# Performance work log

Hardware: AMD Instinct MI355X
Metric: run time of the kernel (lower is better)

Reference implementation:

```python
import jax, jax.numpy as jnp
import numpy as np


def setup_inputs() -> dict:
    key = jax.random.key(0)
    ks = jax.random.split(key, 6)
    B, S, D, E = 4, 2048, 1024, 8
    H = 4 * D
    return {
        "x": jax.random.normal(ks[0], (B, S, D), dtype=jnp.float32),
        "logits": jax.random.normal(ks[1], (B, S, E), dtype=jnp.float32),
        "noise": jax.random.normal(ks[2], (B, S, E), dtype=jnp.float32),
        "W1": jax.random.normal(ks[3], (E, D, H), dtype=jnp.float32) * (1.0 / np.sqrt(D)),
        "b1": jnp.zeros((E, H), dtype=jnp.float32),
        "W2": jax.random.normal(ks[4], (E, H, D), dtype=jnp.float32) * (1.0 / np.sqrt(H)),
        "b2": jnp.zeros((E, D), dtype=jnp.float32),
        "top_k": 2,
    }


def reference(x, logits, noise, W1, b1, W2, b2, top_k):
    # NoisyTopkRouter_Cluster: noise scaled by softplus(logits), then sparse top-k softmax
    B, S, D = x.shape
    E = logits.shape[-1]
    noisy = logits + noise * jax.nn.softplus(logits)           # [B,S,E]
    _, topi = jax.lax.top_k(noisy, top_k)                      # [B,S,K]
    in_topk = jax.nn.one_hot(topi, E, dtype=jnp.bool_).any(-2)  # [B,S,E]
    sparse = jnp.where(in_topk, noisy, -jnp.inf)
    gates = jax.nn.softmax(sparse, axis=-1)                    # [B,S,E]; zero off top-k

    # SparseMoE combine: sum_e gate[:, e] * Expert_e(x). Gate is exactly 0 for
    # unselected experts, so dense-masked compute matches the gather/scatter loop.
    xf = x.reshape(-1, D)                                      # [T,D]
    gf = gates.reshape(-1, E).T                                # [E,T]

    def body(acc, params):
        w1, bb1, w2, bb2, g = params                           # g: [T]
        h = jax.nn.relu(xf @ w1 + bb1)                         # [T,4D]
        acc = acc + (h @ w2 + bb2) * g[:, None]
        return acc, None

    acc, _ = jax.lax.scan(body, jnp.zeros_like(xf), (W1, b1, W2, b2, gf))
    return acc.reshape(B, S, D)
```

## Files before the change

kernel.cpp:

```cpp
#include <hip/hip_runtime.h>
#include <cstdint>
#include <cstddef>

#define T_TOK 8192
#define E_NUM 8
#define D_DIM 1024
#define H_DIM 4096
#define MAXTILES 136
#define TILE 128
#define BK 32

typedef __attribute__((ext_vector_type(8))) short short8;
typedef __attribute__((ext_vector_type(4))) float f32x4;
typedef __attribute__((ext_vector_type(8))) unsigned short ushort8v;
typedef __attribute__((ext_vector_type(4))) unsigned short ushort4v;

__device__ __forceinline__ unsigned short f2b(float f) {
  unsigned int u = __float_as_uint(f);
  u += 0x7fffu + ((u >> 16) & 1u);
  return (unsigned short)(u >> 16);
}

__device__ __forceinline__ void async16(const void* g, void* l) {
  __builtin_amdgcn_global_load_lds((const __attribute__((address_space(1))) void*)g,
                                   (__attribute__((address_space(3))) void*)l, 16, 0, 0);
}

__global__ void router_kernel(const float* __restrict__ logits, const float* __restrict__ noise,
                              int* __restrict__ counts, int* __restrict__ ti, float* __restrict__ tg) {
  int tk = blockIdx.x * blockDim.x + threadIdx.x;
  if (tk >= T_TOK) return;
  float nz[E_NUM];
#pragma unroll
  for (int e = 0; e < E_NUM; ++e) {
    float l = logits[tk * E_NUM + e];
    float sp = fmaxf(l, 0.f) + log1pf(expf(-fabsf(l)));
    nz[e] = l + noise[tk * E_NUM + e] * sp;
  }
  int i1 = 0; float v1 = nz[0];
#pragma unroll
  for (int e = 1; e < E_NUM; ++e) if (nz[e] > v1) { v1 = nz[e]; i1 = e; }
  int i2 = -1; float v2 = -3.0e38f;
#pragma unroll
  for (int e = 0; e < E_NUM; ++e) if (e != i1 && nz[e] > v2) { v2 = nz[e]; i2 = e; }
  float ex = expf(v2 - v1);
  float g1 = 1.f / (1.f + ex);
  float g2 = ex / (1.f + ex);
  int s1 = atomicAdd(&counts[i1], 1);
  int s2 = atomicAdd(&counts[i2], 1);
  ti[tk*4+0] = i1; ti[tk*4+1] = s1; ti[tk*4+2] = i2; ti[tk*4+3] = s2;
  tg[tk*2+0] = g1; tg[tk*2+1] = g2;
}

__global__ void setup_kernel(const int* __restrict__ counts, int* __restrict__ offs,
                             int* __restrict__ tab) {
  int o = 0;
  for (int e = 0; e < E_NUM; ++e) { offs[e] = o; o += counts[e]; }
  offs[E_NUM] = o;
  int mt = 0;
  for (int e = 0; e < E_NUM; ++e)
    for (int m0 = 0; m0 < counts[e]; m0 += TILE) { tab[mt*2] = e; tab[mt*2+1] = m0; ++mt; }
  for (; mt < MAXTILES; ++mt) { tab[mt*2] = -1; tab[mt*2+1] = 0; }
}

__global__ void gather_kernel(const float* __restrict__ x, const int* __restrict__ ti,
                              const float* __restrict__ tg, const int* __restrict__ offs,
                              unsigned short* __restrict__ xg, int* __restrict__ stok,
                              float* __restrict__ sg) {
  const int tk = blockIdx.x, t = threadIdx.x;
  const int i1 = ti[tk*4+0], s1 = ti[tk*4+1], i2 = ti[tk*4+2], s2 = ti[tk*4+3];
  const int r1 = offs[i1] + s1, r2 = offs[i2] + s2;
  if (t == 0) {
    stok[r1] = tk; sg[r1] = tg[tk*2+0];
    stok[r2] = tk; sg[r2] = tg[tk*2+1];
  }
  const float4 v = *(const float4*)(x + (size_t)tk * D_DIM + t * 4);
  ushort4v bb; bb.x = f2b(v.x); bb.y = f2b(v.y); bb.z = f2b(v.z); bb.w = f2b(v.w);
  *(ushort4v*)(xg + (size_t)r1 * D_DIM + t * 4) = bb;
  *(ushort4v*)(xg + (size_t)r2 * D_DIM + t * 4) = bb;
}

__global__ void transpose_kernel(const float* __restrict__ W, unsigned short* __restrict__ Wt,
                                 int K, int N) {
  const int e = blockIdx.z;
  const float* We = W + (size_t)e * K * N;
  unsigned short* Wte = Wt + (size_t)e * K * N;
  __shared__ __align__(16) unsigned short tb[64 * 72];
  const int n0 = blockIdx.x * 64, k0 = blockIdx.y * 64;
  const int t = threadIdx.x;
  const int kr = t >> 4;
  const int c4 = (t & 15) * 4;
#pragma unroll
  for (int rr = 0; rr < 4; ++rr) {
    int k = kr + rr * 16;
    const float4 v = *(const float4*)(We + (size_t)(k0 + k) * N + n0 + c4);
    tb[(c4+0)*72 + k] = f2b(v.x);
    tb[(c4+1)*72 + k] = f2b(v.y);
    tb[(c4+2)*72 + k] = f2b(v.z);
    tb[(c4+3)*72 + k] = f2b(v.w);
  }
  __syncthreads();
  const int n = t >> 2, kq = (t & 3) * 16;
  ushort8v a = *(const ushort8v*)&tb[n*72 + kq];
  ushort8v b = *(const ushort8v*)&tb[n*72 + kq + 8];
  *(ushort8v*)(Wte + (size_t)(n0+n)*K + k0 + kq) = a;
  *(ushort8v*)(Wte + (size_t)(n0+n)*K + k0 + kq + 8) = b;
}

template<int EPI>
__global__ __launch_bounds__(256)
void gemm_bt(const unsigned short* __restrict__ A, const unsigned short* __restrict__ Bt,
             const int K, const int N,
             const int* __restrict__ counts, const int* __restrict__ offs,
             const int* __restrict__ tab,
             const float* __restrict__ bias,
             unsigned short* __restrict__ Hout,
             float* __restrict__ Out,
             const int* __restrict__ slot_tok, const float* __restrict__ slot_gate) {
  const int mt = blockIdx.y;
  const int e = tab[mt*2];
  if (e < 0) return;
  const int m0  = tab[mt*2+1];
  const int cnt = counts[e];
  const int seg = offs[e];
  const int n0  = blockIdx.x * TILE;

  __shared__ __align__(16) short As[TILE*BK];
  __shared__ __align__(16) short Bs[TILE*BK];
  __shared__ int   s_tok[TILE];
  __shared__ float s_g[TILE];

  const int t = threadIdx.x;
  const int lane = t & 63;
  const int wv = t >> 6;
  const int wm = wv & 1, wn = wv >> 1;
  const int fr = lane & 15, fq = lane >> 4;

  if (EPI == 1 && t < TILE) {
    int rl = m0 + t;
    if (rl < cnt) { s_tok[t] = slot_tok[seg + rl]; s_g[t] = slot_gate[seg + rl]; }
    else          { s_tok[t] = 0;                  s_g[t] = 0.f; }
  }

  const unsigned short* Ae = A + (size_t)seg * K;
  const unsigned short* Be = Bt + (size_t)e * N * K + (size_t)n0 * K;

  const int row0 = t >> 2;
  const int kq0  = (t & 3) * 8;
  int ar0 = m0 + row0;        ar0 = ar0 < cnt ? ar0 : cnt - 1;
  int ar1 = m0 + row0 + 64;   ar1 = ar1 < cnt ? ar1 : cnt - 1;
  const unsigned short* gA0 = Ae + (size_t)ar0 * K + kq0;
  const unsigned short* gA1 = Ae + (size_t)ar1 * K + kq0;
  const unsigned short* gB0 = Be + (size_t)row0 * K + kq0;
  const unsigned short* gB1 = Be + (size_t)(row0 + 64) * K + kq0;
  char* lA0 = (char*)As + wv*1024;
  char* lA1 = (char*)As + 4096 + wv*1024;
  char* lB0 = (char*)Bs + wv*1024;
  char* lB1 = (char*)Bs + 4096 + wv*1024;

  f32x4 acc[4][4];
#pragma unroll
  for (int i = 0; i < 4; ++i)
#pragma unroll
    for (int j = 0; j < 4; ++j) acc[i][j] = (f32x4){0.f, 0.f, 0.f, 0.f};

  for (int k0 = 0; k0 < K; k0 += BK) {
    async16(gA0, lA0); async16(gA1, lA1);
    async16(gB0, lB0); async16(gB1, lB1);
    gA0 += BK; gA1 += BK; gB0 += BK; gB1 += BK;
    asm volatile("s_waitcnt vmcnt(0)" ::: "memory");
    __syncthreads();

    short8 af[4], bf[4];
#pragma unroll
    for (int i = 0; i < 4; ++i) af[i] = *(const short8*)&As[(wm*64 + i*16 + fr)*BK + fq*8];
#pragma unroll
    for (int j = 0; j < 4; ++j) bf[j] = *(const short8*)&Bs[(wn*64 + j*16 + fr)*BK + fq*8];
#pragma unroll
    for (int i = 0; i < 4; ++i)
#pragma unroll
      for (int j = 0; j < 4; ++j)
        acc[i][j] = __builtin_amdgcn_mfma_f32_16x16x32_bf16(af[i], bf[j], acc[i][j], 0, 0, 0);
    __syncthreads();
  }

  if (EPI == 0) {
    const float* be = bias + (size_t)e * N;
#pragma unroll
    for (int j = 0; j < 4; ++j) {
      int col = n0 + wn*64 + j*16 + fr;
      float bv = be[col];
#pragma unroll
      for (int i = 0; i < 4; ++i) {
        int rb = m0 + wm*64 + i*16 + fq*4;
#pragma unroll
        for (int r = 0; r < 4; ++r) {
          int rl = rb + r;
          if (rl < cnt) {
            float v = acc[i][j][r] + bv;
            v = v > 0.f ? v : 0.f;
            Hout[(size_t)(seg + rl) * N + col] = f2b(v);
          }
        }
      }
    }
  } else {
    const float* be = bias + (size_t)e * N;
#pragma unroll
    for (int j = 0; j < 4; ++j) {
      int col = n0 + wn*64 + j*16 + fr;
      float bv = be[col];
#pragma unroll
      for (int i = 0; i < 4; ++i) {
        int rbt = wm*64 + i*16 + fq*4;
#pragma unroll
        for (int r = 0; r < 4; ++r) {
          int rlt = rbt + r;
          if (m0 + rlt < cnt) {
            float v = (acc[i][j][r] + bv) * s_g[rlt];
            unsafeAtomicAdd(Out + (size_t)s_tok[rlt] * N + col, v);
          }
        }
      }
    }
  }
}

extern "C" void kernel_launch(void* const* d_in, const int* in_sizes, int n_in,
                              void* d_out, int out_size, void* d_ws, size_t ws_size,
                              hipStream_t stream) {
  const float* x      = (const float*)d_in[0];
  const float* logits = (const float*)d_in[1];
  const float* noise  = (const float*)d_in[2];
  const float* W1     = (const float*)d_in[3];
  const float* b1     = (const float*)d_in[4];
  const float* W2     = (const float*)d_in[5];
  const float* b2     = (const float*)d_in[6];
  float* out = (float*)d_out;

  char* ws = (char*)d_ws;
  size_t off = 0;
  auto alloc = [&](size_t b) { size_t o = off; off = (off + b + 255) & ~(size_t)255; return o; };
  size_t o_counts = alloc(E_NUM * 4);
  size_t o_offs   = alloc((E_NUM + 1) * 4);
  size_t o_tab    = alloc((size_t)MAXTILES * 2 * 4);
  size_t o_ti     = alloc((size_t)T_TOK * 4 * 4);
  size_t o_tg     = alloc((size_t)T_TOK * 2 * 4);
  size_t o_stok   = alloc((size_t)2 * T_TOK * 4);
  size_t o_sg     = alloc((size_t)2 * T_TOK * 4);
  size_t o_xg     = alloc((size_t)2 * T_TOK * D_DIM * 2);
  size_t o_w1t    = alloc((size_t)E_NUM * D_DIM * H_DIM * 2);
  size_t o_w2t    = alloc((size_t)E_NUM * D_DIM * H_DIM * 2);
  size_t o_h      = alloc((size_t)2 * T_TOK * H_DIM * 2);
  if (off > ws_size) return;

  int*            counts = (int*)(ws + o_counts);
  int*            offsp  = (int*)(ws + o_offs);
  int*            tab    = (int*)(ws + o_tab);
  int*            ti     = (int*)(ws + o_ti);
  float*          tg     = (float*)(ws + o_tg);
  int*            stok   = (int*)(ws + o_stok);
  float*          sg     = (float*)(ws + o_sg);
  unsigned short* xg     = (unsigned short*)(ws + o_xg);
  unsigned short* w1t    = (unsigned short*)(ws + o_w1t);
  unsigned short* w2t    = (unsigned short*)(ws + o_w2t);
  unsigned short* h      = (unsigned short*)(ws + o_h);

  hipMemsetAsync(out, 0, (size_t)out_size * sizeof(float), stream);
  hipMemsetAsync(counts, 0, E_NUM * sizeof(int), stream);

  router_kernel<<<T_TOK / 256, 256, 0, stream>>>(logits, noise, counts, ti, tg);
  setup_kernel<<<1, 1, 0, stream>>>(counts, offsp, tab);
  gather_kernel<<<T_TOK, 256, 0, stream>>>(x, ti, tg, offsp, xg, stok, sg);

  transpose_kernel<<<dim3(H_DIM/64, D_DIM/64, E_NUM), 256, 0, stream>>>(W1, w1t, D_DIM, H_DIM);
  transpose_kernel<<<dim3(D_DIM/64, H_DIM/64, E_NUM), 256, 0, stream>>>(W2, w2t, H_DIM, D_DIM);

  gemm_bt<0><<<dim3(H_DIM/TILE, MAXTILES), 256, 0, stream>>>(
      xg, w1t, D_DIM, H_DIM, counts, offsp, tab, b1, h, nullptr, nullptr, nullptr);
  gemm_bt<1><<<dim3(D_DIM/TILE, MAXTILES), 256, 0, stream>>>(
      h, w2t, H_DIM, D_DIM, counts, offsp, tab, b2, nullptr, out, stok, sg);
}
```

Before: 998.6 us.

## Swizzle LDS K-chunks and remap GEMM blocks for XCD-local weight reuse

The two GEMM kernels move to a 1D grid whose block index is remapped so that consecutive blocks (round-robined across the 8 XCDs) share N-column groups. Each XCD then works on a contiguous slice of weight columns across M tiles, which should improve L2 reuse of the expert weights. The LDS layout of A and B tiles is also XOR-swizzled per row on the 16-byte K chunk, to reduce bank conflicts on the MFMA fragment reads. The global source address is swizzled to match the direct-to-LDS async load. This adds index arithmetic and assumes NX is a multiple of 8.

```diff
diff --git a/kernel.cpp b/kernel.cpp
--- a/kernel.cpp
+++ b/kernel.cpp
@@ -107,7 +107,7 @@
   *(ushort8v*)(Wte + (size_t)(n0+n)*K + k0 + kq + 8) = b;
 }
 
-template<int EPI>
+template<int EPI, int NX>
 __global__ __launch_bounds__(256)
 void gemm_bt(const unsigned short* __restrict__ A, const unsigned short* __restrict__ Bt,
              const int K, const int N,
@@ -117,13 +117,19 @@
              unsigned short* __restrict__ Hout,
              float* __restrict__ Out,
              const int* __restrict__ slot_tok, const float* __restrict__ slot_gate) {
-  const int mt = blockIdx.y;
+  constexpr int G = NX / 8;
+  const int bid = blockIdx.x;
+  const int c = bid & 7;
+  const int s = bid >> 3;
+  const int xi = c * G + (s % G);
+  const int mt = s / G;
+
   const int e = tab[mt*2];
   if (e < 0) return;
   const int m0  = tab[mt*2+1];
   const int cnt = counts[e];
   const int seg = offs[e];
-  const int n0  = blockIdx.x * TILE;
+  const int n0  = xi * TILE;
 
   __shared__ __align__(16) short As[TILE*BK];
   __shared__ __align__(16) short Bs[TILE*BK];
@@ -146,13 +152,13 @@
   const unsigned short* Be = Bt + (size_t)e * N * K + (size_t)n0 * K;
 
   const int row0 = t >> 2;
-  const int kq0  = (t & 3) * 8;
+  const int kcg  = ((t & 3) ^ (row0 & 3)) * 8;
   int ar0 = m0 + row0;        ar0 = ar0 < cnt ? ar0 : cnt - 1;
   int ar1 = m0 + row0 + 64;   ar1 = ar1 < cnt ? ar1 : cnt - 1;
-  const unsigned short* gA0 = Ae + (size_t)ar0 * K + kq0;
-  const unsigned short* gA1 = Ae + (size_t)ar1 * K + kq0;
-  const unsigned short* gB0 = Be + (size_t)row0 * K + kq0;
-  const unsigned short* gB1 = Be + (size_t)(row0 + 64) * K + kq0;
+  const unsigned short* gA0 = Ae + (size_t)ar0 * K + kcg;
+  const unsigned short* gA1 = Ae + (size_t)ar1 * K + kcg;
+  const unsigned short* gB0 = Be + (size_t)row0 * K + kcg;
+  const unsigned short* gB1 = Be + (size_t)(row0 + 64) * K + kcg;
   char* lA0 = (char*)As + wv*1024;
   char* lA1 = (char*)As + 4096 + wv*1024;
   char* lB0 = (char*)Bs + wv*1024;
@@ -173,9 +179,15 @@
 
     short8 af[4], bf[4];
 #pragma unroll
-    for (int i = 0; i < 4; ++i) af[i] = *(const short8*)&As[(wm*64 + i*16 + fr)*BK + fq*8];
-#pragma unroll
-    for (int j = 0; j < 4; ++j) bf[j] = *(const short8*)&Bs[(wn*64 + j*16 + fr)*BK + fq*8];
+    for (int i = 0; i < 4; ++i) {
+      int row = wm*64 + i*16 + fr;
+      af[i] = *(const short8*)&As[row*BK + (fq ^ (row & 3))*8];
+    }
+#pragma unroll
+    for (int j = 0; j < 4; ++j) {
+      int row = wn*64 + j*16 + fr;
+      bf[j] = *(const short8*)&Bs[row*BK + (fq ^ (row & 3))*8];
+    }
 #pragma unroll
     for (int i = 0; i < 4; ++i)
 #pragma unroll
@@ -276,8 +288,8 @@
   transpose_kernel<<<dim3(H_DIM/64, D_DIM/64, E_NUM), 256, 0, stream>>>(W1, w1t, D_DIM, H_DIM);
   transpose_kernel<<<dim3(D_DIM/64, H_DIM/64, E_NUM), 256, 0, stream>>>(W2, w2t, H_DIM, D_DIM);
 
-  gemm_bt<0><<<dim3(H_DIM/TILE, MAXTILES), 256, 0, stream>>>(
+  gemm_bt<0, H_DIM/TILE><<<dim3((H_DIM/TILE) * MAXTILES), 256, 0, stream>>>(
       xg, w1t, D_DIM, H_DIM, counts, offsp, tab, b1, h, nullptr, nullptr, nullptr);
-  gemm_bt<1><<<dim3(D_DIM/TILE, MAXTILES), 256, 0, stream>>>(
+  gemm_bt<1, D_DIM/TILE><<<dim3((D_DIM/TILE) * MAXTILES), 256, 0, stream>>>(
       h, w2t, H_DIM, D_DIM, counts, offsp, tab, b2, nullptr, out, stok, sg);
 }
```

After: 999.4 us. Within noise of the previous version (+0.1%).
